# Kernel optimization log

Hardware: AMD Instinct MI355X
Metric: run time of the kernel (lower is better)

The kernel has to match this reference:

```python
import jax, jax.numpy as jnp
import numpy as np

C = 256
NUM_HEADS = 8
HEAD_DIM = C // NUM_HEADS
GROUPS = min(32, C // 4)
EPS = 1e-5


def setup_inputs() -> dict:
    key = jax.random.key(0)
    ks = jax.random.split(key, 6)
    B, H, W = 8, 32, 32
    x = jax.random.normal(ks[0], (B, C, H, W), dtype=jnp.float32)
    gn_w = jnp.ones((C,), jnp.float32)
    gn_b = jnp.zeros((C,), jnp.float32)
    qkv_w = jax.random.normal(ks[1], (3 * C, C), jnp.float32) * (1.0 / np.sqrt(C))
    qkv_b = jnp.zeros((3 * C,), jnp.float32)
    proj_w = jax.random.normal(ks[2], (C, C), jnp.float32) * (1.0 / np.sqrt(C))
    proj_b = jnp.zeros((C,), jnp.float32)
    return {"x": x, "gn_w": gn_w, "gn_b": gn_b, "qkv_w": qkv_w,
            "qkv_b": qkv_b, "proj_w": proj_w, "proj_b": proj_b}


def _group_norm(x, w, b):
    B, Cc, H, W = x.shape
    xg = x.reshape(B, GROUPS, Cc // GROUPS, H * W)
    mu = xg.mean(axis=(2, 3), keepdims=True)
    var = xg.var(axis=(2, 3), keepdims=True)
    xn = (xg - mu) * jax.lax.rsqrt(var + EPS)
    xn = xn.reshape(B, Cc, H, W)
    return xn * w[None, :, None, None] + b[None, :, None, None]


def reference(x, gn_w, gn_b, qkv_w, qkv_b, proj_w, proj_b):
    B, Cc, H, W = x.shape
    N = H * W
    h = _group_norm(x, gn_w, gn_b)
    h = h.reshape(B, Cc, N)
    # 1x1 conv == channel matmul
    qkv = jnp.einsum('oc,bcn->bon', qkv_w, h) + qkv_b[None, :, None]
    qkv = qkv.reshape(B, 3, NUM_HEADS, HEAD_DIM, N)
    q, k, v = qkv[:, 0], qkv[:, 1], qkv[:, 2]
    scale = HEAD_DIM ** -0.5
    attn = jnp.einsum('bhdi,bhdj->bhij', q, k) * scale  # (B,h,N,N)
    attn = jax.nn.softmax(attn, axis=-1)
    out = jnp.einsum('bhij,bhdj->bhdi', attn, v)  # (B,h,d,N)
    out = out.reshape(B, Cc, H, W)
    out = jnp.einsum('oc,bchw->bohw', proj_w, out) + proj_b[None, :, None, None]
    return x + out
```

## Files before the change

### kernel.cpp

```cpp
#include <hip/hip_runtime.h>
#include <hip/hip_bf16.h>

#define B_ 8
#define C_ 256
#define N_ 1024
#define NH 8

#define SL 0.25507675857f

using bf16x8 = __attribute__((ext_vector_type(8))) short;
using s16x4  = __attribute__((ext_vector_type(4))) short;
using f32x4  = __attribute__((ext_vector_type(4))) float;

__device__ inline short f2bf(float f) {
  union { float f; unsigned u; } v; v.f = f;
  unsigned r = v.u + 0x7fffu + ((v.u >> 16) & 1u);
  return (short)(r >> 16);
}

__device__ inline int cvt_pk_bf16(float lo, float hi) {
  int r;
  asm("v_cvt_pk_bf16_f32 %0, %1, %2" : "=v"(r) : "v"(lo), "v"(hi));
  return r;
}

__global__ __launch_bounds__(256) void pre_kernel(const float* __restrict__ wq,
    const float* __restrict__ wp, short* __restrict__ wbf,
    const float* __restrict__ x, const float* __restrict__ gw,
    const float* __restrict__ gb, short* __restrict__ h_t)
{
  __shared__ float smem[8];
  const int bid = blockIdx.x;
  if (bid < 1024) {
    const int i = bid * 256 + threadIdx.x;
    if (i < 65536)       wbf[i] = f2bf(wq[i] * SL);
    else if (i < 196608) wbf[i] = f2bf(wq[i]);
    else                 wbf[i] = f2bf(wp[i - 196608]);
    return;
  }
  const int bb = (bid - 1024) & 7;
  const int g  = (bid - 1024) >> 3;
  const size_t base = ((size_t)bb * C_ + g * 8) * N_;
  const float* xp = x + base;

  float vals[32];
  float sum = 0.f, sq = 0.f;
#pragma unroll
  for (int r = 0; r < 32; ++r) {
    float v = xp[r * 256 + threadIdx.x];
    vals[r] = v; sum += v; sq += v * v;
  }
#pragma unroll
  for (int off = 32; off; off >>= 1) {
    sum += __shfl_down(sum, off);
    sq  += __shfl_down(sq,  off);
  }
  const int wid = threadIdx.x >> 6;
  if ((threadIdx.x & 63) == 0) { smem[wid] = sum; smem[4 + wid] = sq; }
  __syncthreads();
  sum = smem[0] + smem[1] + smem[2] + smem[3];
  sq  = smem[4] + smem[5] + smem[6] + smem[7];

  const float mu  = sum * (1.f / 8192.f);
  const float var = sq  * (1.f / 8192.f) - mu * mu;
  const float rs  = rsqrtf(var + 1e-5f);

#pragma unroll
  for (int qn = 0; qn < 4; ++qn) {
    short tmp[8];
#pragma unroll
    for (int ch = 0; ch < 8; ++ch) {
      const int cc = g * 8 + ch;
      tmp[ch] = f2bf((vals[ch * 4 + qn] - mu) * rs * gw[cc] + gb[cc]);
    }
    *(bf16x8*)&h_t[((size_t)bb * N_ + qn * 256 + threadIdx.x) * C_ + g * 8] = *(bf16x8*)tmp;
  }
}

template<int MODE, int BN>
__device__ __forceinline__ void gemm_body(int b, int by, int bz,
    const short* __restrict__ Aw, const short* __restrict__ Bw,
    const float* __restrict__ bias, const float* __restrict__ resid,
    void* __restrict__ Cout)
{
  constexpr int NI = BN / 32;
  const short* A  = (MODE == 0) ? Aw + (size_t)b * N_ * C_ : Aw;
  const short* Bp = (MODE == 0) ? Bw : Bw + (size_t)b * N_ * C_;

  const int tid = threadIdx.x;
  const int lane = tid & 63, wid = tid >> 6;
  const int g = lane >> 4, c = lane & 15;
  const int wm = wid >> 1, wn = wid & 1;
  const int m0 = by * 64, n0 = bz * BN;

  __shared__ short At[64][72];
  __shared__ short Bt[BN][72];

  const int srow = tid >> 3, sseg = tid & 7;
  bf16x8 areg[2], breg[NI];
#pragma unroll
  for (int j = 0; j < 2; ++j)
    areg[j] = *(const bf16x8*)&A[(size_t)(m0 + srow + j * 32) * 256 + sseg * 8];
#pragma unroll
  for (int j = 0; j < NI; ++j)
    breg[j] = *(const bf16x8*)&Bp[(size_t)(n0 + srow + j * 32) * 256 + sseg * 8];

  f32x4 acc[2][NI] = {};

  for (int kb = 0; kb < 256; kb += 64) {
    __syncthreads();
#pragma unroll
    for (int j = 0; j < 2; ++j) *(bf16x8*)&At[srow + j * 32][sseg * 8] = areg[j];
#pragma unroll
    for (int j = 0; j < NI; ++j) *(bf16x8*)&Bt[srow + j * 32][sseg * 8] = breg[j];
    __syncthreads();

    if (kb < 192) {
      const int kn = kb + 64;
#pragma unroll
      for (int j = 0; j < 2; ++j)
        areg[j] = *(const bf16x8*)&A[(size_t)(m0 + srow + j * 32) * 256 + kn + sseg * 8];
#pragma unroll
      for (int j = 0; j < NI; ++j)
        breg[j] = *(const bf16x8*)&Bp[(size_t)(n0 + srow + j * 32) * 256 + kn + sseg * 8];
    }

#pragma unroll
    for (int kk = 0; kk < 2; ++kk) {
      bf16x8 af[2], bfr[NI];
#pragma unroll
      for (int mi = 0; mi < 2; ++mi)
        af[mi] = *(const bf16x8*)&At[wm * 32 + mi * 16 + c][kk * 32 + g * 8];
#pragma unroll
      for (int ni = 0; ni < NI; ++ni)
        bfr[ni] = *(const bf16x8*)&Bt[wn * (BN / 2) + ni * 16 + c][kk * 32 + g * 8];
#pragma unroll
      for (int mi = 0; mi < 2; ++mi)
#pragma unroll
        for (int ni = 0; ni < NI; ++ni)
          acc[mi][ni] = __builtin_amdgcn_mfma_f32_16x16x32_bf16(af[mi], bfr[ni],
                                                                acc[mi][ni], 0, 0, 0);
    }
  }

#pragma unroll
  for (int mi = 0; mi < 2; ++mi)
#pragma unroll
    for (int ni = 0; ni < NI; ++ni) {
      const int col = n0 + wn * (BN / 2) + ni * 16 + c;
#pragma unroll
      for (int r = 0; r < 4; ++r) {
        const int row = m0 + wm * 32 + mi * 16 + g * 4 + r;
        float v = acc[mi][ni][r];
        if (MODE == 0) {
          v += (col < 256) ? bias[col] * SL : bias[col];
          ((short*)Cout)[((size_t)b * N_ + row) * 512 + col] = f2bf(v);
        } else if (MODE == 1) {
          v += bias[row];
          ((short*)Cout)[((size_t)b * 256 + row) * N_ + col] = f2bf(v);
        } else {
          v += bias[row] + resid[((size_t)b * 256 + row) * N_ + col];
          ((float*)Cout)[((size_t)b * 256 + row) * N_ + col] = v;
        }
      }
    }
}

__global__ __launch_bounds__(256) void qkv_kernel(const short* __restrict__ h_t,
    const short* __restrict__ wbf, const float* __restrict__ qkv_b,
    short* __restrict__ qk_t, short* __restrict__ v_sep)
{
  const int bid = blockIdx.x;
  if (bid < 512)
    gemm_body<0, 128>(bid & 7, (bid >> 3) & 15, bid >> 7, h_t, wbf, qkv_b, nullptr, qk_t);
  else {
    const int b2 = bid - 512;
    gemm_body<1, 64>(b2 & 7, (b2 >> 3) & 3, b2 >> 5, wbf + 512 * 256, h_t,
                     qkv_b + 512, nullptr, v_sep);
  }
}

__global__ __launch_bounds__(256) void proj_kernel(const short* __restrict__ wbf,
    const short* __restrict__ att_t, const float* __restrict__ pj_b,
    const float* __restrict__ x, float* __restrict__ out)
{
  const int bid = blockIdx.x;
  gemm_body<2, 64>(bid & 7, (bid >> 3) & 3, bid >> 5, wbf + 768 * 256, att_t, pj_b, x, out);
}

__global__ __launch_bounds__(256) void attn_mfma(const short* __restrict__ qkt,
    const short* __restrict__ v_sep, short* __restrict__ att_t)
{
  const int bh = blockIdx.x;
  const int b = bh >> 3, hh = bh & 7;
  const int tid  = threadIdx.x;
  const int w    = tid >> 6;
  const int qhalf = w >> 1, kvh = w & 1;
  const int lane = tid & 63;
  const int g = lane >> 4, c = lane & 15;
  const int q0 = blockIdx.y * 128 + qhalf * 64;

  const short* qk_b = qkt + (size_t)b * N_ * 512;
  const short* v_b  = v_sep + ((size_t)b * 256 + hh * 32) * N_;

  bf16x8 qb[4];
#pragma unroll
  for (int m = 0; m < 4; ++m)
    qb[m] = *(const bf16x8*)&qk_b[(size_t)(q0 + m * 16 + c) * 512 + hh * 32 + g * 8];

  const short* kp[4];
#pragma unroll
  for (int kc = 0; kc < 4; ++kc) {
    const int krow = (kc & 1) * 32 + (c >> 2) * 8 + ((kc >> 1) << 2) + (c & 3);
    kp[kc] = qk_b + (size_t)krow * 512 + 256 + hh * 32 + g * 8;
  }
  const short* vpA = v_b + (size_t)c * N_ + g * 8;
  const short* vpB = v_b + (size_t)(16 + c) * N_ + g * 8;

  f32x4 acc[4][2] = {};
  float lsum[4] = {0.f, 0.f, 0.f, 0.f};
  const f32x4 cinit = {-16.f, -16.f, -16.f, -16.f};

  const int t0 = kvh * 8;
  bf16x8 kf[4], vv[4];
#pragma unroll
  for (int kc = 0; kc < 4; ++kc)
    kf[kc] = *(const bf16x8*)(kp[kc] + (size_t)t0 * 64 * 512);
  vv[0] = *(const bf16x8*)(vpA + t0 * 64);
  vv[1] = *(const bf16x8*)(vpA + t0 * 64 + 32);
  vv[2] = *(const bf16x8*)(vpB + t0 * 64);
  vv[3] = *(const bf16x8*)(vpB + t0 * 64 + 32);

  for (int ii = 0; ii < 8; ++ii) {
    const int kt = t0 + ii;
    int pk[4][4][2];
#pragma unroll
    for (int m = 0; m < 4; ++m) {
      f32x4 s[4];
      __builtin_amdgcn_s_setprio(1);
#pragma unroll
      for (int kc = 0; kc < 4; ++kc)
        s[kc] = __builtin_amdgcn_mfma_f32_16x16x32_bf16(kf[kc], qb[m], cinit, 0, 0, 0);
      __builtin_amdgcn_s_setprio(0);
      float sum = 0.f;
#pragma unroll
      for (int kc = 0; kc < 4; ++kc) {
#pragma unroll
        for (int r = 0; r < 4; ++r) {
          s[kc][r] = __builtin_amdgcn_exp2f(s[kc][r]);
          sum += s[kc][r];
        }
        pk[m][kc][0] = cvt_pk_bf16(s[kc][0], s[kc][1]);
        pk[m][kc][1] = cvt_pk_bf16(s[kc][2], s[kc][3]);
      }
      lsum[m] += sum;
    }

    if (ii < 7) {
#pragma unroll
      for (int kc = 0; kc < 4; ++kc)
        kf[kc] = *(const bf16x8*)(kp[kc] + (size_t)(kt + 1) * 64 * 512);
    }

    __builtin_amdgcn_s_setprio(1);
#pragma unroll
    for (int m = 0; m < 4; ++m)
#pragma unroll
      for (int ks = 0; ks < 2; ++ks) {
        union { bf16x8 v; int i[4]; } pb;
        pb.i[0] = pk[m][ks][0];
        pb.i[1] = pk[m][ks][1];
        pb.i[2] = pk[m][ks + 2][0];
        pb.i[3] = pk[m][ks + 2][1];
        acc[m][0] = __builtin_amdgcn_mfma_f32_16x16x32_bf16(ks ? vv[1] : vv[0], pb.v,
                                                            acc[m][0], 0, 0, 0);
        acc[m][1] = __builtin_amdgcn_mfma_f32_16x16x32_bf16(ks ? vv[3] : vv[2], pb.v,
                                                            acc[m][1], 0, 0, 0);
      }
    __builtin_amdgcn_s_setprio(0);

    if (ii < 7) {
      vv[0] = *(const bf16x8*)(vpA + (kt + 1) * 64);
      vv[1] = *(const bf16x8*)(vpA + (kt + 1) * 64 + 32);
      vv[2] = *(const bf16x8*)(vpB + (kt + 1) * 64);
      vv[3] = *(const bf16x8*)(vpB + (kt + 1) * 64 + 32);
    }
  }

#pragma unroll
  for (int m = 0; m < 4; ++m) {
    lsum[m] += __shfl_xor(lsum[m], 16);
    lsum[m] += __shfl_xor(lsum[m], 32);
  }

  __shared__ float xls[2][64][37];
  if (kvh == 1) {
#pragma unroll
    for (int m = 0; m < 4; ++m) {
#pragma unroll
      for (int dd = 0; dd < 2; ++dd)
#pragma unroll
        for (int r = 0; r < 4; ++r)
          xls[qhalf][lane][m * 8 + dd * 4 + r] = acc[m][dd][r];
      xls[qhalf][lane][32 + m] = lsum[m];
    }
  }
  __syncthreads();
  if (kvh == 0) {
#pragma unroll
    for (int m = 0; m < 4; ++m) {
      const float l = lsum[m] + xls[qhalf][lane][32 + m];
      const float inv = 1.f / l;
      const int q = q0 + m * 16 + c;
#pragma unroll
      for (int dd = 0; dd < 2; ++dd) {
        short st[4];
#pragma unroll
        for (int r = 0; r < 4; ++r)
          st[r] = f2bf((acc[m][dd][r] + xls[qhalf][lane][m * 8 + dd * 4 + r]) * inv);
        *(s16x4*)&att_t[((size_t)b * N_ + q) * C_ + hh * 32 + dd * 16 + g * 4] = *(s16x4*)st;
      }
    }
  }
}

extern "C" void kernel_launch(void* const* d_in, const int* in_sizes, int n_in,
                              void* d_out, int out_size, void* d_ws, size_t ws_size,
                              hipStream_t stream)
{
  const float* x     = (const float*)d_in[0];
  const float* gn_w  = (const float*)d_in[1];
  const float* gn_b  = (const float*)d_in[2];
  const float* qkv_w = (const float*)d_in[3];
  const float* qkv_b = (const float*)d_in[4];
  const float* pj_w  = (const float*)d_in[5];
  const float* pj_b  = (const float*)d_in[6];
  float* out = (float*)d_out;

  short* h_t   = (short*)d_ws;
  short* qk_t  = h_t   + (size_t)B_ * N_ * C_;
  short* v_sep = qk_t  + (size_t)B_ * N_ * 512;
  short* att_t = v_sep + (size_t)B_ * C_ * N_;
  short* wbf   = att_t + (size_t)B_ * N_ * C_;

  pre_kernel <<<1280, 256, 0, stream>>>(qkv_w, pj_w, wbf, x, gn_w, gn_b, h_t);
  qkv_kernel <<<1024, 256, 0, stream>>>(h_t, wbf, qkv_b, qk_t, v_sep);
  attn_mfma  <<<dim3(B_ * NH, 8), 256, 0, stream>>>(qk_t, v_sep, att_t);
  proj_kernel<<<512,  256, 0, stream>>>(wbf, att_t, pj_b, x, out);
}
```

Measured before the change: 47.26 us.

## Split attention KV range four ways per block, each wave covering all 128 queries

Before, each block of four waves split work as two query halves times two KV halves. Now each wave handles all 128 queries and a quarter of the KV tiles, and three waves' partial accumulators and row sums are reduced through shared memory by wave 0. The QK exp and PV MFMAs are interleaved per 16-query subtile, with the next K/V loads issued mid-loop. This halves per-wave K/V loads relative to the query work, at the cost of doubled accumulator registers, a larger LDS reduction and a serial final pass done by a single wave.

```diff
diff --git a/kernel.cpp b/kernel.cpp
--- a/kernel.cpp
+++ b/kernel.cpp
@@ -193,19 +193,19 @@
 {
   const int bh = blockIdx.x;
   const int b = bh >> 3, hh = bh & 7;
+  const int q0 = blockIdx.y * 128;
+
   const int tid  = threadIdx.x;
   const int w    = tid >> 6;
-  const int qhalf = w >> 1, kvh = w & 1;
   const int lane = tid & 63;
   const int g = lane >> 4, c = lane & 15;
-  const int q0 = blockIdx.y * 128 + qhalf * 64;
 
   const short* qk_b = qkt + (size_t)b * N_ * 512;
   const short* v_b  = v_sep + ((size_t)b * 256 + hh * 32) * N_;
 
-  bf16x8 qb[4];
-#pragma unroll
-  for (int m = 0; m < 4; ++m)
+  bf16x8 qb[8];
+#pragma unroll
+  for (int m = 0; m < 8; ++m)
     qb[m] = *(const bf16x8*)&qk_b[(size_t)(q0 + m * 16 + c) * 512 + hh * 32 + g * 8];
 
   const short* kp[4];
@@ -217,11 +217,11 @@
   const short* vpA = v_b + (size_t)c * N_ + g * 8;
   const short* vpB = v_b + (size_t)(16 + c) * N_ + g * 8;
 
-  f32x4 acc[4][2] = {};
-  float lsum[4] = {0.f, 0.f, 0.f, 0.f};
+  f32x4 acc[8][2] = {};
+  float lsum[8] = {0.f, 0.f, 0.f, 0.f, 0.f, 0.f, 0.f, 0.f};
   const f32x4 cinit = {-16.f, -16.f, -16.f, -16.f};
 
-  const int t0 = kvh * 8;
+  const int t0 = w * 4;
   bf16x8 kf[4], vv[4];
 #pragma unroll
   for (int kc = 0; kc < 4; ++kc)
@@ -231,18 +231,25 @@
   vv[2] = *(const bf16x8*)(vpB + t0 * 64);
   vv[3] = *(const bf16x8*)(vpB + t0 * 64 + 32);
 
-  for (int ii = 0; ii < 8; ++ii) {
+  for (int ii = 0; ii < 4; ++ii) {
     const int kt = t0 + ii;
-    int pk[4][4][2];
-#pragma unroll
-    for (int m = 0; m < 4; ++m) {
+#pragma unroll
+    for (int m = 0; m < 8; ++m) {
       f32x4 s[4];
       __builtin_amdgcn_s_setprio(1);
 #pragma unroll
       for (int kc = 0; kc < 4; ++kc)
         s[kc] = __builtin_amdgcn_mfma_f32_16x16x32_bf16(kf[kc], qb[m], cinit, 0, 0, 0);
       __builtin_amdgcn_s_setprio(0);
+
+      if (m == 7 && ii < 3) {
+#pragma unroll
+        for (int kc = 0; kc < 4; ++kc)
+          kf[kc] = *(const bf16x8*)(kp[kc] + (size_t)(kt + 1) * 64 * 512);
+      }
+
       float sum = 0.f;
+      int pk[4][2];
 #pragma unroll
       for (int kc = 0; kc < 4; ++kc) {
 #pragma unroll
@@ -250,74 +257,76 @@
           s[kc][r] = __builtin_amdgcn_exp2f(s[kc][r]);
           sum += s[kc][r];
         }
-        pk[m][kc][0] = cvt_pk_bf16(s[kc][0], s[kc][1]);
-        pk[m][kc][1] = cvt_pk_bf16(s[kc][2], s[kc][3]);
+        pk[kc][0] = cvt_pk_bf16(s[kc][0], s[kc][1]);
+        pk[kc][1] = cvt_pk_bf16(s[kc][2], s[kc][3]);
       }
       lsum[m] += sum;
-    }
-
-    if (ii < 7) {
-#pragma unroll
-      for (int kc = 0; kc < 4; ++kc)
-        kf[kc] = *(const bf16x8*)(kp[kc] + (size_t)(kt + 1) * 64 * 512);
-    }
-
-    __builtin_amdgcn_s_setprio(1);
-#pragma unroll
-    for (int m = 0; m < 4; ++m)
+
+      __builtin_amdgcn_s_setprio(1);
 #pragma unroll
       for (int ks = 0; ks < 2; ++ks) {
         union { bf16x8 v; int i[4]; } pb;
-        pb.i[0] = pk[m][ks][0];
-        pb.i[1] = pk[m][ks][1];
-        pb.i[2] = pk[m][ks + 2][0];
-        pb.i[3] = pk[m][ks + 2][1];
+        pb.i[0] = pk[ks][0];
+        pb.i[1] = pk[ks][1];
+        pb.i[2] = pk[ks + 2][0];
+        pb.i[3] = pk[ks + 2][1];
         acc[m][0] = __builtin_amdgcn_mfma_f32_16x16x32_bf16(ks ? vv[1] : vv[0], pb.v,
                                                             acc[m][0], 0, 0, 0);
         acc[m][1] = __builtin_amdgcn_mfma_f32_16x16x32_bf16(ks ? vv[3] : vv[2], pb.v,
                                                             acc[m][1], 0, 0, 0);
       }
-    __builtin_amdgcn_s_setprio(0);
-
-    if (ii < 7) {
-      vv[0] = *(const bf16x8*)(vpA + (kt + 1) * 64);
-      vv[1] = *(const bf16x8*)(vpA + (kt + 1) * 64 + 32);
-      vv[2] = *(const bf16x8*)(vpB + (kt + 1) * 64);
-      vv[3] = *(const bf16x8*)(vpB + (kt + 1) * 64 + 32);
-    }
-  }
-
-#pragma unroll
-  for (int m = 0; m < 4; ++m) {
+      __builtin_amdgcn_s_setprio(0);
+
+      if (m == 7 && ii < 3) {
+        vv[0] = *(const bf16x8*)(vpA + (kt + 1) * 64);
+        vv[1] = *(const bf16x8*)(vpA + (kt + 1) * 64 + 32);
+        vv[2] = *(const bf16x8*)(vpB + (kt + 1) * 64);
+        vv[3] = *(const bf16x8*)(vpB + (kt + 1) * 64 + 32);
+      }
+    }
+  }
+
+#pragma unroll
+  for (int m = 0; m < 8; ++m) {
     lsum[m] += __shfl_xor(lsum[m], 16);
     lsum[m] += __shfl_xor(lsum[m], 32);
   }
 
-  __shared__ float xls[2][64][37];
-  if (kvh == 1) {
-#pragma unroll
-    for (int m = 0; m < 4; ++m) {
-#pragma unroll
-      for (int dd = 0; dd < 2; ++dd)
-#pragma unroll
-        for (int r = 0; r < 4; ++r)
-          xls[qhalf][lane][m * 8 + dd * 4 + r] = acc[m][dd][r];
-      xls[qhalf][lane][32 + m] = lsum[m];
-    }
+  __shared__ float xls[3][64][76];
+  if (w != 0) {
+    float* row = &xls[w - 1][lane][0];
+#pragma unroll
+    for (int m = 0; m < 8; ++m) {
+      *(f32x4*)&row[m * 8]     = acc[m][0];
+      *(f32x4*)&row[m * 8 + 4] = acc[m][1];
+    }
+    *(f32x4*)&row[64] = (f32x4){lsum[0], lsum[1], lsum[2], lsum[3]};
+    *(f32x4*)&row[68] = (f32x4){lsum[4], lsum[5], lsum[6], lsum[7]};
   }
   __syncthreads();
-  if (kvh == 0) {
-#pragma unroll
-    for (int m = 0; m < 4; ++m) {
-      const float l = lsum[m] + xls[qhalf][lane][32 + m];
-      const float inv = 1.f / l;
+  if (w == 0) {
+#pragma unroll
+    for (int p = 0; p < 3; ++p) {
+      const float* row = &xls[p][lane][0];
+#pragma unroll
+      for (int m = 0; m < 8; ++m) {
+        acc[m][0] += *(const f32x4*)&row[m * 8];
+        acc[m][1] += *(const f32x4*)&row[m * 8 + 4];
+      }
+      const f32x4 l0 = *(const f32x4*)&row[64];
+      const f32x4 l1 = *(const f32x4*)&row[68];
+#pragma unroll
+      for (int j = 0; j < 4; ++j) { lsum[j] += l0[j]; lsum[4 + j] += l1[j]; }
+    }
+#pragma unroll
+    for (int m = 0; m < 8; ++m) {
+      const float inv = 1.f / lsum[m];
       const int q = q0 + m * 16 + c;
 #pragma unroll
       for (int dd = 0; dd < 2; ++dd) {
         short st[4];
 #pragma unroll
-        for (int r = 0; r < 4; ++r)
-          st[r] = f2bf((acc[m][dd][r] + xls[qhalf][lane][m * 8 + dd * 4 + r]) * inv);
+        for (int r = 0; r < 4; ++r) st[r] = f2bf(acc[m][dd][r] * inv);
         *(s16x4*)&att_t[((size_t)b * N_ + q) * C_ + hh * 32 + dd * 16 + g * 4] = *(s16x4*)st;
       }
     }
```

Measured after the change: 52.40 us. 10.9% more time.
